# Optimization experiments

Measured on AMD Instinct MI355X. Metric: run time of the kernel, lower is better.

## Reference

```python
import jax, jax.numpy as jnp
import numpy as np

N = 50000      # nodes
E = 800000     # edges (avg degree 16)
F_IN = 512     # num_feature
H = 256        # nhid


def setup_inputs() -> dict:
    key = jax.random.key(0)
    ks = jax.random.split(key, 40)
    def p(k, shape):
        return jax.random.normal(k, shape, jnp.float32) * 0.05
    inp = {}
    inp["x"] = jax.random.normal(ks[0], (N, F_IN), jnp.float32)
    src = jax.random.randint(ks[1], (E,), 0, N, jnp.int32)
    dst = jax.random.randint(ks[2], (E,), 0, N, jnp.int32)
    inp["edge_index"] = jnp.stack([src, dst])  # [2, E]
    # GIN conv MLPs: Lin(din,H), ReLU, Lin(H,H). Weights stored [in, out].
    dims = [F_IN, H, H, H]
    i = 3
    for li, din in enumerate(dims, 1):
        inp[f"c{li}w1"] = p(ks[i], (din, H)); i += 1
        inp[f"c{li}b1"] = p(ks[i], (H,)); i += 1
        inp[f"c{li}w2"] = p(ks[i], (H, H)); i += 1
        inp[f"c{li}b2"] = p(ks[i], (H,)); i += 1
    # 2-layer LSTM, gate order i,f,g,o; single fused bias (b_ih + b_hh).
    for l in range(2):
        inp[f"lstm{l}_wih"] = p(ks[i], (H, 4 * H)); i += 1
        inp[f"lstm{l}_whh"] = p(ks[i], (H, 4 * H)); i += 1
        inp[f"lstm{l}_b"] = p(ks[i], (4 * H,)); i += 1
    inp["mlp_w"] = p(ks[i], (H, H)); i += 1
    inp["mlp_b"] = p(ks[i], (H,))
    return inp


def _gin(h, src, dst, w1, b1, w2, b2):
    # GINConv with eps=0: nn(x + sum_{j->i} x_j)
    agg = jax.ops.segment_sum(h[src], dst, num_segments=N)
    z = jax.nn.relu((h + agg) @ w1 + b1)
    return z @ w2 + b2


def _lstm_layer(seq, wih, whh, b):
    # seq: [T, N, H] -> hidden states [T, N, H]
    def step(carry, xt):
        h, c = carry
        g = xt @ wih + h @ whh + b
        i, f, gg, o = jnp.split(g, 4, axis=-1)
        c = jax.nn.sigmoid(f) * c + jax.nn.sigmoid(i) * jnp.tanh(gg)
        h = jax.nn.sigmoid(o) * jnp.tanh(c)
        return (h, c), h
    h0 = jnp.zeros((seq.shape[1], whh.shape[0]), seq.dtype)
    _, hs = jax.lax.scan(step, (h0, h0), seq)
    return hs


def reference(x, edge_index, c1w1, c1b1, c1w2, c1b2, c2w1, c2b1, c2w2, c2b2,
              c3w1, c3b1, c3w2, c3b2, c4w1, c4b1, c4w2, c4b2,
              lstm0_wih, lstm0_whh, lstm0_b, lstm1_wih, lstm1_whh, lstm1_b,
              mlp_w, mlp_b):
    src, dst = edge_index[0], edge_index[1]
    x1 = jax.nn.relu(_gin(x, src, dst, c1w1, c1b1, c1w2, c1b2))
    x2 = jax.nn.relu(_gin(x1, src, dst, c2w1, c2b1, c2w2, c2b2))
    x3 = jax.nn.relu(_gin(x2, src, dst, c3w1, c3b1, c3w2, c3b2))
    x4 = jax.nn.relu(_gin(x3, src, dst, c4w1, c4b1, c4w2, c4b2))
    # residual sums (in-place cascade as in the original)
    x2 = x2 + x1
    x3 = x3 + x2
    x4 = x4 + x3
    x_sum = x1 + x2 + x3 + x4
    stack = jnp.stack([x_sum, x1, x2, x3, x4])  # [5, N, H]
    x_avg = stack.mean(axis=0)
    x_max = stack.max(axis=0)
    seq = jnp.stack([x1, x2, x3, x4])  # [4, N, H]
    h = _lstm_layer(seq, lstm0_wih, lstm0_whh, lstm0_b)
    h = _lstm_layer(h, lstm1_wih, lstm1_whh, lstm1_b)
    x_lstm = h.mean(axis=0)
    # channel attention: relu(mlp(x_avg) + mlp(x_max) + mlp(x_lstm))
    return jax.nn.relu((x_avg + x_max + x_lstm) @ mlp_w + 3.0 * mlp_b)
```

## Files before the change

### kernel.cpp

```cpp
#include <hip/hip_runtime.h>

typedef unsigned int u32;
typedef unsigned short u16;

typedef __attribute__((ext_vector_type(8))) __bf16 bf16x8;
typedef __attribute__((ext_vector_type(4))) float f32x4;

__device__ __forceinline__ u16 f2bf(float f) {
  u32 u = __float_as_uint(f);
  u += 0x7fffu + ((u >> 16) & 1u);
  return (u16)(u >> 16);
}
__device__ __forceinline__ float bl(u32 u) { return __uint_as_float(u << 16); }
__device__ __forceinline__ float bh(u32 u) { return __uint_as_float(u & 0xffff0000u); }
__device__ __forceinline__ u32 pk2(float a, float b) { return (u32)f2bf(a) | ((u32)f2bf(b) << 16); }
__device__ __forceinline__ float fsig(float x) { return 1.f / (1.f + __expf(-x)); }
__device__ __forceinline__ float ftanh(float x) { return 1.f - 2.f / (__expf(2.f * x) + 1.f); }

#define GLDS16(gp, lp)                                                                  \
  __builtin_amdgcn_global_load_lds((const __attribute__((address_space(1))) u32*)(gp),  \
                                   (__attribute__((address_space(3))) u32*)(lp), 16, 0, 0)

struct WTargs {
  const float* src[13];
  u16* dst[13];
  int K[13];
  int Nc[13];
  int bstart[14];
};
__global__ __launch_bounds__(256) void k_wtall(WTargs wa) {
  int b = blockIdx.x;
  int w = 0;
  while (b >= wa.bstart[w + 1]) ++w;
  int i = (b - wa.bstart[w]) * 256 + threadIdx.x;
  int K = wa.K[w], Nc = wa.Nc[w];
  if (i >= K * Nc) return;
  int k = i / Nc, c = i - k * Nc;
  wa.dst[w][(size_t)c * K + k] = f2bf(wa.src[w][i]);
}

__global__ __launch_bounds__(256) void k_x2bf(const float* __restrict__ x, u16* __restrict__ xb, int total8) {
  int i = blockIdx.x * 256 + threadIdx.x;
  if (i >= total8) return;
  size_t o = (size_t)i * 8;
  float4 a = *(const float4*)(x + o), b = *(const float4*)(x + o + 4);
  uint4 v;
  v.x = pk2(a.x, a.y); v.y = pk2(a.z, a.w); v.z = pk2(b.x, b.y); v.w = pk2(b.z, b.w);
  *(uint4*)(xb + o) = v;
}

__global__ void k_hist(const int* __restrict__ dst, int* __restrict__ deg, int E) {
  int e = blockIdx.x * 256 + threadIdx.x;
  if (e < E) atomicAdd(&deg[dst[e]], 1);
}
__global__ __launch_bounds__(1024) void k_scan1(const int* __restrict__ deg, int* __restrict__ rs,
                                                int* __restrict__ bsum, int n) {
  __shared__ int buf[1024];
  int t = threadIdx.x, idx = blockIdx.x * 1024 + t;
  int v = idx < n ? deg[idx] : 0;
  buf[t] = v;
  __syncthreads();
  for (int off = 1; off < 1024; off <<= 1) {
    int u = t >= off ? buf[t - off] : 0;
    __syncthreads();
    buf[t] += u;
    __syncthreads();
  }
  if (idx < n) rs[idx + 1] = buf[t];
  if (t == 1023) bsum[blockIdx.x] = buf[1023];
}
__global__ void k_scan2(int* bsum, int nb) {
  if (threadIdx.x == 0) {
    int s = 0;
    for (int b = 0; b < nb; ++b) { s += bsum[b]; bsum[b] = s; }
  }
}
__global__ void k_scan3(const int* __restrict__ bsum, int* __restrict__ rs,
                        int* __restrict__ cursor, int n) {
  int i = blockIdx.x * 256 + threadIdx.x;
  if (i >= n) return;
  int b = i >> 10;
  int add = b ? bsum[b - 1] : 0;
  int v = rs[i + 1] + add;
  int d = cursor[i];
  rs[i + 1] = v;
  cursor[i] = v - d;
  if (i == 0) rs[0] = 0;
}
__global__ void k_scatter(const int* __restrict__ src, const int* __restrict__ dst,
                          int* __restrict__ cursor, int* __restrict__ esrc, int E) {
  int e = blockIdx.x * 256 + threadIdx.x;
  if (e < E) {
    int p = atomicAdd(&cursor[dst[e]], 1);
    esrc[p] = src[e];
  }
}

__global__ __launch_bounds__(256) void k_aggbr(const u16* __restrict__ y, const int* __restrict__ rowstart,
                                               const int* __restrict__ esrc, const float* __restrict__ b1,
                                               u16* __restrict__ z, int Nn, int base, int rows) {
  int lane = threadIdx.x & 63, wid = threadIdx.x >> 6;
  int r = blockIdx.x * 4 + wid;
  if (r >= rows) return;
  int node = base + r;
  const int cb = lane * 4;
  u16* orow = z + (size_t)r * 256 + cb;
  if (node >= Nn) { *(uint2*)orow = uint2{0, 0}; return; }
  float acc[4];
  {
    uint2 v = *(const uint2*)(y + (size_t)node * 256 + cb);
    acc[0] = bl(v.x); acc[1] = bh(v.x); acc[2] = bl(v.y); acc[3] = bh(v.y);
  }
  int s = rowstart[node], e = rowstart[node + 1];
  int j = s;
  for (; j + 3 < e; j += 4) {
    uint2 v0 = *(const uint2*)(y + (size_t)esrc[j] * 256 + cb);
    uint2 v1 = *(const uint2*)(y + (size_t)esrc[j + 1] * 256 + cb);
    uint2 v2 = *(const uint2*)(y + (size_t)esrc[j + 2] * 256 + cb);
    uint2 v3 = *(const uint2*)(y + (size_t)esrc[j + 3] * 256 + cb);
    acc[0] += (bl(v0.x) + bl(v1.x)) + (bl(v2.x) + bl(v3.x));
    acc[1] += (bh(v0.x) + bh(v1.x)) + (bh(v2.x) + bh(v3.x));
    acc[2] += (bl(v0.y) + bl(v1.y)) + (bl(v2.y) + bl(v3.y));
    acc[3] += (bh(v0.y) + bh(v1.y)) + (bh(v2.y) + bh(v3.y));
  }
  for (; j < e; ++j) {
    uint2 v = *(const uint2*)(y + (size_t)esrc[j] * 256 + cb);
    acc[0] += bl(v.x); acc[1] += bh(v.x); acc[2] += bl(v.y); acc[3] += bh(v.y);
  }
  float4 bb = *(const float4*)(b1 + cb);
  acc[0] = fmaxf(acc[0] + bb.x, 0.f);
  acc[1] = fmaxf(acc[1] + bb.y, 0.f);
  acc[2] = fmaxf(acc[2] + bb.z, 0.f);
  acc[3] = fmaxf(acc[3] + bb.w, 0.f);
  uint2 o;
  o.x = pk2(acc[0], acc[1]); o.y = pk2(acc[2], acc[3]);
  *(uint2*)orow = o;
}

__global__ __launch_bounds__(256) void k_agg256(const u16* __restrict__ h,
                                                const int* __restrict__ rowstart,
                                                const int* __restrict__ esrc,
                                                u16* __restrict__ out, int Nn, int base, int rows) {
  int lane = threadIdx.x & 63, wid = threadIdx.x >> 6;
  int r = blockIdx.x * 4 + wid;
  if (r >= rows) return;
  int node = base + r;
  const int cb = lane * 4;
  u16* orow = out + (size_t)r * 256 + cb;
  if (node >= Nn) { *(uint2*)orow = uint2{0, 0}; return; }
  float acc[4];
  {
    uint2 v = *(const uint2*)(h + (size_t)node * 256 + cb);
    acc[0] = bl(v.x); acc[1] = bh(v.x); acc[2] = bl(v.y); acc[3] = bh(v.y);
  }
  int s = rowstart[node], e = rowstart[node + 1];
  int j = s;
  for (; j + 3 < e; j += 4) {
    uint2 v0 = *(const uint2*)(h + (size_t)esrc[j] * 256 + cb);
    uint2 v1 = *(const uint2*)(h + (size_t)esrc[j + 1] * 256 + cb);
    uint2 v2 = *(const uint2*)(h + (size_t)esrc[j + 2] * 256 + cb);
    uint2 v3 = *(const uint2*)(h + (size_t)esrc[j + 3] * 256 + cb);
    acc[0] += (bl(v0.x) + bl(v1.x)) + (bl(v2.x) + bl(v3.x));
    acc[1] += (bh(v0.x) + bh(v1.x)) + (bh(v2.x) + bh(v3.x));
    acc[2] += (bl(v0.y) + bl(v1.y)) + (bl(v2.y) + bl(v3.y));
    acc[3] += (bh(v0.y) + bh(v1.y)) + (bh(v2.y) + bh(v3.y));
  }
  for (; j < e; ++j) {
    uint2 v = *(const uint2*)(h + (size_t)esrc[j] * 256 + cb);
    acc[0] += bl(v.x); acc[1] += bh(v.x); acc[2] += bl(v.y); acc[3] += bh(v.y);
  }
  uint2 o;
  o.x = pk2(acc[0], acc[1]); o.y = pk2(acc[2], acc[3]);
  *(uint2*)orow = o;
}

template <int BN, int MODE>
__global__ __launch_bounds__(256) void k_gemm(const u16* __restrict__ A1, const u16* __restrict__ B1, int K1,
                                              const u16* __restrict__ A2, const u16* __restrict__ B2, int K2,
                                              const float* __restrict__ bias, float bscale,
                                              void* __restrict__ outp, int Nout, int Mstore, int NT,
                                              u16* __restrict__ cstp, float* __restrict__ hsump,
                                              int first, int dosum) {
  constexpr int NF = BN / 32;
  __shared__ u16 Al[128 * 64];
  __shared__ u16 Bl[BN * 64];
  const int tid = threadIdx.x;
  const int lane = tid & 63, wid = tid >> 6;
  const int wr = wid >> 1, wc = wid & 1;
  const int nwg = gridDim.x;
  const int orig = blockIdx.x;
  const int q = nwg >> 3, rr8 = nwg & 7;
  const int xcd = orig & 7;
  const int wgid = (xcd < rr8 ? xcd * (q + 1) : rr8 * (q + 1) + (xcd - rr8) * q) + (orig >> 3);
  const int mtile = wgid / NT, ntile = wgid - mtile * NT;
  const int m0 = mtile * 128;
  const int n0 = ntile * BN;
  const int h0 = ntile * 32;
  const int l15 = lane & 15, l4 = lane >> 4;
  const int srow = lane >> 3;
  const int scol = ((lane & 7) ^ (lane >> 3)) * 8;
  const int rsw = l15 & 7;
  f32x4 acc[4][NF] = {};

  for (int s = 0; s < 2; ++s) {
    const u16* A = s ? A2 : A1;
    const u16* B = s ? B2 : B1;
    const int K = s ? K2 : K1;
    if (A == nullptr) continue;
    for (int k0 = 0; k0 < K; k0 += 64) {
      __syncthreads();
#pragma unroll
      for (int p = 0; p < 4; ++p) {
        int r = m0 + p * 32 + wid * 8 + srow;
        GLDS16(A + (size_t)r * K + k0 + scol, &Al[(p * 32 + wid * 8) * 64]);
      }
#pragma unroll
      for (int p = 0; p < NF; ++p) {
        int r;
        if constexpr (MODE == 3) r = p * 256 + h0 + wid * 8 + srow;
        else r = n0 + p * 32 + wid * 8 + srow;
        GLDS16(B + (size_t)r * K + k0 + scol, &Bl[(p * 32 + wid * 8) * 64]);
      }
      __syncthreads();
#pragma unroll
      for (int ks = 0; ks < 2; ++ks) {
        const int sp = (((ks * 4 + l4) ^ rsw)) * 8;
        bf16x8 af[4], bfr[NF];
#pragma unroll
        for (int m = 0; m < 4; ++m)
          af[m] = *(const bf16x8*)&Al[(wr * 64 + m * 16 + l15) * 64 + sp];
#pragma unroll
        for (int n = 0; n < NF; ++n) {
          int trow;
          if constexpr (MODE == 3) trow = n * 32 + wc * 16 + l15;
          else trow = wc * (BN / 2) + n * 16 + l15;
          bfr[n] = *(const bf16x8*)&Bl[trow * 64 + sp];
        }
#pragma unroll
        for (int m = 0; m < 4; ++m)
#pragma unroll
          for (int n = 0; n < NF; ++n)
            acc[m][n] = __builtin_amdgcn_mfma_f32_16x16x32_bf16(af[m], bfr[n], acc[m][n], 0, 0, 0);
      }
    }
  }

  if constexpr (MODE == 3) {
    const int hcol = h0 + wc * 16 + l15;
    const float bi = bias[hcol], bf2 = bias[256 + hcol];
    const float bg = bias[512 + hcol], bo = bias[768 + hcol];
    u16* hout = (u16*)outp;
#pragma unroll
    for (int m = 0; m < 4; ++m) {
      int gr0 = m0 + wr * 64 + m * 16 + l4 * 4;
#pragma unroll
      for (int r = 0; r < 4; ++r) {
        int gr = gr0 + r;
        if (gr >= Mstore) continue;
        float gi = acc[m][0][r] + bi;
        float gf = acc[m][1][r] + bf2;
        float gg = acc[m][2][r] + bg;
        float go = acc[m][3][r] + bo;
        size_t o = (size_t)gr * 256 + hcol;
        float nc = fsig(gi) * ftanh(gg);
        if (!first) nc += fsig(gf) * bl((u32)cstp[o]);
        cstp[o] = f2bf(nc);
        nc = bl((u32)f2bf(nc));
        float h = fsig(go) * ftanh(nc);
        hout[o] = f2bf(h);
        if (dosum) {
          if (first) hsump[o] = h;
          else hsump[o] += h;
        }
      }
    }
    return;
  }

#pragma unroll
  for (int m = 0; m < 4; ++m) {
    int gr0 = m0 + wr * 64 + m * 16 + l4 * 4;
#pragma unroll
    for (int n = 0; n < NF; ++n) {
      int gc = n0 + wc * (BN / 2) + n * 16 + l15;
      float bb = bias ? bias[gc] * bscale : 0.f;
#pragma unroll
      for (int r = 0; r < 4; ++r) {
        int gr = gr0 + r;
        if (gr >= Mstore) continue;
        float v = acc[m][n][r] + bb;
        if (MODE >= 1) v = fmaxf(v, 0.f);
        if (MODE == 2) ((float*)outp)[(size_t)gr * Nout + gc] = v;
        else ((u16*)outp)[(size_t)gr * Nout + gc] = f2bf(v);
      }
    }
  }
}

__global__ __launch_bounds__(256) void k_cascade(const u16* __restrict__ x1, u16* __restrict__ x2,
                                                 u16* __restrict__ x3, u16* __restrict__ x4, int total4) {
  int i = blockIdx.x * 256 + threadIdx.x;
  if (i >= total4) return;
  size_t o = (size_t)i * 4;
  uint2 v1 = *(const uint2*)(x1 + o), v2 = *(const uint2*)(x2 + o);
  uint2 v3 = *(const uint2*)(x3 + o), v4 = *(const uint2*)(x4 + o);
  float a1[4] = {bl(v1.x), bh(v1.x), bl(v1.y), bh(v1.y)};
  float a2[4] = {bl(v2.x), bh(v2.x), bl(v2.y), bh(v2.y)};
  float a3[4] = {bl(v3.x), bh(v3.x), bl(v3.y), bh(v3.y)};
  float a4[4] = {bl(v4.x), bh(v4.x), bl(v4.y), bh(v4.y)};
  float y2[4], y3[4], y4[4];
#pragma unroll
  for (int j = 0; j < 4; ++j) {
    y2[j] = a2[j] + a1[j];
    y3[j] = a3[j] + y2[j];
    y4[j] = a4[j] + y3[j];
  }
  *(uint2*)(x2 + o) = uint2{pk2(y2[0], y2[1]), pk2(y2[2], y2[3])};
  *(uint2*)(x3 + o) = uint2{pk2(y3[0], y3[1]), pk2(y3[2], y3[3])};
  *(uint2*)(x4 + o) = uint2{pk2(y4[0], y4[1]), pk2(y4[2], y4[3])};
}

__global__ __launch_bounds__(256) void k_sfin(const u16* __restrict__ x1, const u16* __restrict__ x2,
                                              const u16* __restrict__ x3, const u16* __restrict__ x4,
                                              const float* __restrict__ hsum, u16* __restrict__ sb,
                                              int total4) {
  int i = blockIdx.x * 256 + threadIdx.x;
  if (i >= total4) return;
  size_t o = (size_t)i * 4;
  uint2 v1 = *(const uint2*)(x1 + o), v2 = *(const uint2*)(x2 + o);
  uint2 v3 = *(const uint2*)(x3 + o), v4 = *(const uint2*)(x4 + o);
  float4 hh = *(const float4*)(hsum + o);
  float r0 = 1.4f * (bl(v1.x) + bl(v2.x) + bl(v3.x) + bl(v4.x)) + 0.25f * hh.x;
  float r1 = 1.4f * (bh(v1.x) + bh(v2.x) + bh(v3.x) + bh(v4.x)) + 0.25f * hh.y;
  float r2 = 1.4f * (bl(v1.y) + bl(v2.y) + bl(v3.y) + bl(v4.y)) + 0.25f * hh.z;
  float r3 = 1.4f * (bh(v1.y) + bh(v2.y) + bh(v3.y) + bh(v4.y)) + 0.25f * hh.w;
  *(uint2*)(sb + o) = uint2{pk2(r0, r1), pk2(r2, r3)};
}

extern "C" void kernel_launch(void* const* d_in, const int* in_sizes, int n_in,
                              void* d_out, int out_size, void* d_ws, size_t ws_size,
                              hipStream_t stream) {
  (void)n_in; (void)out_size;
  const int N = in_sizes[0] / 512;
  const int E = in_sizes[1] / 2;
  const int Mpad = ((N + 127) / 128) * 128;
  auto al128 = [](int v) { return ((v + 127) / 128) * 128; };

  const float* x = (const float*)d_in[0];
  const int* ei = (const int*)d_in[1];
  const int* esrc_in = ei;
  const int* edst_in = ei + E;

  size_t off = 0;
  auto alloc = [&](size_t bytes) { size_t o = off; off += (bytes + 255) & ~(size_t)255; return o; };
  char* ws = (char*)d_ws;
  const size_t szH = (size_t)Mpad * 256 * 2;
  const size_t szXB = (size_t)Mpad * 512 * 2;
  const int widx[13] = {2, 4, 6, 8, 10, 12, 14, 16, 18, 19, 21, 22, 24};
  const int wK[13] = {512, 256, 256, 256, 256, 256, 256, 256, 256, 256, 256, 256, 256};
  const int wN[13] = {256, 256, 256, 256, 256, 256, 256, 256, 1024, 1024, 1024, 1024, 256};
  size_t wt_o[13];
  for (int i = 0; i < 13; ++i) wt_o[i] = alloc((size_t)wK[i] * wN[i] * 2);
  size_t rowstart_o = alloc((size_t)(N + 1) * 4);
  size_t cursor_o = alloc((size_t)N * 4);
  size_t bsum_o = alloc(256 * 4);
  size_t esrc_o = alloc((size_t)E * 4);
  size_t x_o[4];
  for (int t = 0; t < 4; ++t) x_o[t] = alloc(szH);
  int McC = al128((Mpad + 3) / 4);
  int McL = al128((Mpad + 7) / 8);
  {
    const int ccand[3] = {Mpad, al128((Mpad + 1) / 2), al128((Mpad + 3) / 4)};
    const int lcand[5] = {Mpad, al128((Mpad + 1) / 2), 16384, 8192, al128((Mpad + 7) / 8)};
    bool done = false;
    for (int ci = 0; ci < 3 && !done; ++ci) {
      for (int li = 0; li < 5 && !done; ++li) {
        size_t cneed = szXB + szH + (size_t)ccand[ci] * 512;
        size_t lneed = (size_t)lcand[li] * 5120;
        size_t tmp = cneed > lneed ? cneed : lneed;
        if (off + tmp + (1u << 20) <= ws_size) { McC = ccand[ci]; McL = lcand[li]; done = true; }
      }
    }
  }
  const size_t hb = (size_t)McL * 256 * 2;
  const size_t fb = (size_t)McL * 256 * 4;
  size_t lstm_sz = 8 * hb + fb;
  size_t conv_sz = szXB + szH + (size_t)McC * 512;
  size_t tmp_o = alloc(lstm_sz > conv_sz ? lstm_sz : conv_sz);
  if (off > ws_size) return;

  u16* wt[13];
  for (int i = 0; i < 13; ++i) wt[i] = (u16*)(ws + wt_o[i]);
  int* rowstart = (int*)(ws + rowstart_o);
  int* cursor = (int*)(ws + cursor_o);
  int* bsum = (int*)(ws + bsum_o);
  int* esrc = (int*)(ws + esrc_o);
  u16* xl[4];
  for (int t = 0; t < 4; ++t) xl[t] = (u16*)(ws + x_o[t]);
  u16* xb = (u16*)(ws + tmp_o);
  u16* y1 = (u16*)(ws + tmp_o + szXB);
  u16* zC = (u16*)(ws + tmp_o + szXB + szH);
  u16* h0s[4];
  for (int t = 0; t < 4; ++t) h0s[t] = (u16*)(ws + tmp_o + t * hb);
  u16* h1p[2] = {(u16*)(ws + tmp_o + 4 * hb), (u16*)(ws + tmp_o + 5 * hb)};
  u16* cst = (u16*)(ws + tmp_o + 6 * hb);
  u16* sbc = (u16*)(ws + tmp_o + 7 * hb);
  float* hsum = (float*)(ws + tmp_o + 8 * hb);

  WTargs wa;
  int bacc = 0;
  for (int i = 0; i < 13; ++i) {
    wa.src[i] = (const float*)d_in[widx[i]];
    wa.dst[i] = wt[i];
    wa.K[i] = wK[i];
    wa.Nc[i] = wN[i];
    wa.bstart[i] = bacc;
    bacc += (wK[i] * wN[i] + 255) / 256;
  }
  wa.bstart[13] = bacc;
  k_wtall<<<bacc, 256, 0, stream>>>(wa);
  k_x2bf<<<(N * 64 + 255) / 256, 256, 0, stream>>>(x, xb, N * 64);
  if (Mpad > N) hipMemsetAsync(xb + (size_t)N * 512, 0, (size_t)(Mpad - N) * 512 * 2, stream);
  hipMemsetAsync(cursor, 0, (size_t)N * 4, stream);
  k_hist<<<(E + 255) / 256, 256, 0, stream>>>(edst_in, cursor, E);
  const int nb = (N + 1023) / 1024;
  k_scan1<<<nb, 1024, 0, stream>>>(cursor, rowstart, bsum, N);
  k_scan2<<<1, 64, 0, stream>>>(bsum, nb);
  k_scan3<<<(N + 255) / 256, 256, 0, stream>>>(bsum, rowstart, cursor, N);
  k_scatter<<<(E + 255) / 256, 256, 0, stream>>>(esrc_in, edst_in, cursor, esrc, E);

  auto gemm = [&](const u16* A1, const u16* B1, int K1, const u16* A2, const u16* B2, int K2,
                  const float* bias, float bscale, void* out, int Nout, int rows, int Mstore,
                  int mode) {
    dim3 b(256);
    if (mode == 0) {
      int NT = Nout / 128;
      dim3 g((rows / 128) * NT);
      k_gemm<128, 0><<<g, b, 0, stream>>>(A1, B1, K1, A2, B2, K2, bias, bscale, out, Nout, Mstore,
                                          NT, nullptr, nullptr, 0, 0);
    } else if (mode == 1) {
      int NT = Nout / 128;
      dim3 g((rows / 128) * NT);
      k_gemm<128, 1><<<g, b, 0, stream>>>(A1, B1, K1, A2, B2, K2, bias, bscale, out, Nout, Mstore,
                                          NT, nullptr, nullptr, 0, 0);
    } else {
      int NT = Nout / 64;
      dim3 g((rows / 128) * NT);
      k_gemm<64, 2><<<g, b, 0, stream>>>(A1, B1, K1, A2, B2, K2, bias, bscale, out, Nout, Mstore,
                                         NT, nullptr, nullptr, 0, 0);
    }
  };
  auto lstm_step = [&](const u16* xt, const u16* wih, const u16* hprev, const u16* whh,
                       const float* bias, u16* hout, float* hsumP, int rows, int first, int dosum) {
    dim3 g((rows / 128) * 8), b(256);
    k_gemm<128, 3><<<g, b, 0, stream>>>(xt, wih, 256, hprev, whh, 256, bias, 1.f,
                                        hout, 256, rows, 8, cst, hsumP, first, dosum);
  };

  gemm(xb, wt[0], 512, nullptr, nullptr, 0, nullptr, 0.f, y1, 256, Mpad, Mpad, 0);
  for (int base = 0; base < Mpad; base += McC) {
    int rows = Mpad - base < McC ? Mpad - base : McC;
    int ab = (rows + 3) / 4;
    k_aggbr<<<ab, 256, 0, stream>>>(y1, rowstart, esrc, (const float*)d_in[3], zC, N, base, rows);
    gemm(zC, wt[1], 256, nullptr, nullptr, 0, (const float*)d_in[5], 1.f,
         xl[0] + (size_t)base * 256, 256, rows, rows, 1);
  }
  for (int l = 1; l < 4; ++l) {
    const int cb1[4] = {3, 7, 11, 15}, cb2[4] = {5, 9, 13, 17};
    for (int base = 0; base < Mpad; base += McC) {
      int rows = Mpad - base < McC ? Mpad - base : McC;
      int ab = (rows + 3) / 4;
      k_agg256<<<ab, 256, 0, stream>>>(xl[l - 1], rowstart, esrc, zC, N, base, rows);
      gemm((u16*)zC, wt[2 * l], 256, nullptr, nullptr, 0, (const float*)d_in[cb1[l]], 1.f,
           y1, 256, rows, rows, 1);
      gemm(y1, wt[2 * l + 1], 256, nullptr, nullptr, 0, (const float*)d_in[cb2[l]], 1.f,
           xl[l] + (size_t)base * 256, 256, rows, rows, 1);
    }
  }
  k_cascade<<<(Mpad * 64 + 255) / 256, 256, 0, stream>>>(xl[0], xl[1], xl[2], xl[3], Mpad * 64);

  const float* b_l0 = (const float*)d_in[20];
  const float* b_l1 = (const float*)d_in[23];
  const float* b_mlp = (const float*)d_in[25];
  for (int base = 0; base < Mpad; base += McL) {
    int rows = Mpad - base < McL ? Mpad - base : McL;
    const size_t boff = (size_t)base * 256;
    for (int t = 0; t < 4; ++t)
      lstm_step(xl[t] + boff, wt[8], t ? h0s[t - 1] : nullptr, wt[9], b_l0,
                h0s[t], nullptr, rows, t == 0, 0);
    for (int t = 0; t < 4; ++t)
      lstm_step(h0s[t], wt[10], t ? h1p[(t + 1) & 1] : nullptr, wt[11], b_l1,
                h1p[t & 1], hsum, rows, t == 0, 1);
    k_sfin<<<(rows * 64 + 255) / 256, 256, 0, stream>>>(xl[0] + boff, xl[1] + boff, xl[2] + boff,
                                                        xl[3] + boff, hsum, sbc, rows * 64);
    int st = N - base;
    if (st > rows) st = rows;
    if (st > 0)
      gemm(sbc, wt[12], 256, nullptr, nullptr, 0, b_mlp, 3.f,
           (float*)d_out + boff, 256, rows, st, 2);
  }
}
```

Measured before the change: 1.436 ms.

## Use 256-row tiles for LSTM gemm, bf16 hidden-sum buffer, larger LSTM chunks

Templates the gemm on the M tile size and runs the fused LSTM step gemm with 256-row tiles, so each weight tile loaded into LDS is reused across twice as many rows. The running LSTM hidden-state sum is stored in bf16 instead of fp32, which cuts its memory traffic and workspace. The LSTM row-chunk candidates are changed to allow larger or full-size chunks, which means fewer launches. The cost is higher register and LDS use per block, lower occupancy, and bf16 rounding on the accumulated hidden sum.

```diff
diff --git a/kernel.cpp b/kernel.cpp
--- a/kernel.cpp
+++ b/kernel.cpp
@@ -174,15 +174,16 @@
   *(uint2*)orow = o;
 }
 
-template <int BN, int MODE>
+template <int BM, int BN, int MODE>
 __global__ __launch_bounds__(256) void k_gemm(const u16* __restrict__ A1, const u16* __restrict__ B1, int K1,
                                               const u16* __restrict__ A2, const u16* __restrict__ B2, int K2,
                                               const float* __restrict__ bias, float bscale,
                                               void* __restrict__ outp, int Nout, int Mstore, int NT,
-                                              u16* __restrict__ cstp, float* __restrict__ hsump,
+                                              u16* __restrict__ cstp, u16* __restrict__ hsump,
                                               int first, int dosum) {
+  constexpr int MF = BM / 32;
   constexpr int NF = BN / 32;
-  __shared__ u16 Al[128 * 64];
+  __shared__ u16 Al[BM * 64];
   __shared__ u16 Bl[BN * 64];
   const int tid = threadIdx.x;
   const int lane = tid & 63, wid = tid >> 6;
@@ -193,14 +194,14 @@
   const int xcd = orig & 7;
   const int wgid = (xcd < rr8 ? xcd * (q + 1) : rr8 * (q + 1) + (xcd - rr8) * q) + (orig >> 3);
   const int mtile = wgid / NT, ntile = wgid - mtile * NT;
-  const int m0 = mtile * 128;
+  const int m0 = mtile * BM;
   const int n0 = ntile * BN;
   const int h0 = ntile * 32;
   const int l15 = lane & 15, l4 = lane >> 4;
   const int srow = lane >> 3;
   const int scol = ((lane & 7) ^ (lane >> 3)) * 8;
   const int rsw = l15 & 7;
-  f32x4 acc[4][NF] = {};
+  f32x4 acc[MF][NF] = {};
 
   for (int s = 0; s < 2; ++s) {
     const u16* A = s ? A2 : A1;
@@ -210,7 +211,7 @@
     for (int k0 = 0; k0 < K; k0 += 64) {
       __syncthreads();
 #pragma unroll
-      for (int p = 0; p < 4; ++p) {
+      for (int p = 0; p < MF; ++p) {
         int r = m0 + p * 32 + wid * 8 + srow;
         GLDS16(A + (size_t)r * K + k0 + scol, &Al[(p * 32 + wid * 8) * 64]);
       }
@@ -225,10 +226,10 @@
 #pragma unroll
       for (int ks = 0; ks < 2; ++ks) {
         const int sp = (((ks * 4 + l4) ^ rsw)) * 8;
-        bf16x8 af[4], bfr[NF];
-#pragma unroll
-        for (int m = 0; m < 4; ++m)
-          af[m] = *(const bf16x8*)&Al[(wr * 64 + m * 16 + l15) * 64 + sp];
+        bf16x8 af[MF], bfr[NF];
+#pragma unroll
+        for (int m = 0; m < MF; ++m)
+          af[m] = *(const bf16x8*)&Al[(wr * (BM / 2) + m * 16 + l15) * 64 + sp];
 #pragma unroll
         for (int n = 0; n < NF; ++n) {
           int trow;
@@ -237,7 +238,7 @@
           bfr[n] = *(const bf16x8*)&Bl[trow * 64 + sp];
         }
 #pragma unroll
-        for (int m = 0; m < 4; ++m)
+        for (int m = 0; m < MF; ++m)
 #pragma unroll
           for (int n = 0; n < NF; ++n)
             acc[m][n] = __builtin_amdgcn_mfma_f32_16x16x32_bf16(af[m], bfr[n], acc[m][n], 0, 0, 0);
@@ -251,8 +252,8 @@
     const float bg = bias[512 + hcol], bo = bias[768 + hcol];
     u16* hout = (u16*)outp;
 #pragma unroll
-    for (int m = 0; m < 4; ++m) {
-      int gr0 = m0 + wr * 64 + m * 16 + l4 * 4;
+    for (int m = 0; m < MF; ++m) {
+      int gr0 = m0 + wr * (BM / 2) + m * 16 + l4 * 4;
 #pragma unroll
       for (int r = 0; r < 4; ++r) {
         int gr = gr0 + r;
@@ -269,8 +270,8 @@
         float h = fsig(go) * ftanh(nc);
         hout[o] = f2bf(h);
         if (dosum) {
-          if (first) hsump[o] = h;
-          else hsump[o] += h;
+          if (first) hsump[o] = f2bf(h);
+          else hsump[o] = f2bf(bl((u32)hsump[o]) + h);
         }
       }
     }
@@ -278,8 +279,8 @@
   }
 
 #pragma unroll
-  for (int m = 0; m < 4; ++m) {
-    int gr0 = m0 + wr * 64 + m * 16 + l4 * 4;
+  for (int m = 0; m < MF; ++m) {
+    int gr0 = m0 + wr * (BM / 2) + m * 16 + l4 * 4;
 #pragma unroll
     for (int n = 0; n < NF; ++n) {
       int gc = n0 + wc * (BN / 2) + n * 16 + l15;
@@ -322,18 +323,19 @@
 
 __global__ __launch_bounds__(256) void k_sfin(const u16* __restrict__ x1, const u16* __restrict__ x2,
                                               const u16* __restrict__ x3, const u16* __restrict__ x4,
-                                              const float* __restrict__ hsum, u16* __restrict__ sb,
+                                              const u16* __restrict__ hsum, u16* __restrict__ sb,
                                               int total4) {
   int i = blockIdx.x * 256 + threadIdx.x;
   if (i >= total4) return;
   size_t o = (size_t)i * 4;
   uint2 v1 = *(const uint2*)(x1 + o), v2 = *(const uint2*)(x2 + o);
   uint2 v3 = *(const uint2*)(x3 + o), v4 = *(const uint2*)(x4 + o);
-  float4 hh = *(const float4*)(hsum + o);
-  float r0 = 1.4f * (bl(v1.x) + bl(v2.x) + bl(v3.x) + bl(v4.x)) + 0.25f * hh.x;
-  float r1 = 1.4f * (bh(v1.x) + bh(v2.x) + bh(v3.x) + bh(v4.x)) + 0.25f * hh.y;
-  float r2 = 1.4f * (bl(v1.y) + bl(v2.y) + bl(v3.y) + bl(v4.y)) + 0.25f * hh.z;
-  float r3 = 1.4f * (bh(v1.y) + bh(v2.y) + bh(v3.y) + bh(v4.y)) + 0.25f * hh.w;
+  uint2 vh = *(const uint2*)(hsum + o);
+  float hh[4] = {bl(vh.x), bh(vh.x), bl(vh.y), bh(vh.y)};
+  float r0 = 1.4f * (bl(v1.x) + bl(v2.x) + bl(v3.x) + bl(v4.x)) + 0.25f * hh[0];
+  float r1 = 1.4f * (bh(v1.x) + bh(v2.x) + bh(v3.x) + bh(v4.x)) + 0.25f * hh[1];
+  float r2 = 1.4f * (bl(v1.y) + bl(v2.y) + bl(v3.y) + bl(v4.y)) + 0.25f * hh[2];
+  float r3 = 1.4f * (bh(v1.y) + bh(v2.y) + bh(v3.y) + bh(v4.y)) + 0.25f * hh[3];
   *(uint2*)(sb + o) = uint2{pk2(r0, r1), pk2(r2, r3)};
 }
 
@@ -343,7 +345,7 @@
   (void)n_in; (void)out_size;
   const int N = in_sizes[0] / 512;
   const int E = in_sizes[1] / 2;
-  const int Mpad = ((N + 127) / 128) * 128;
+  const int Mpad = ((N + 255) / 256) * 256;
   auto al128 = [](int v) { return ((v + 127) / 128) * 128; };
 
   const float* x = (const float*)d_in[0];
@@ -368,23 +370,22 @@
   size_t x_o[4];
   for (int t = 0; t < 4; ++t) x_o[t] = alloc(szH);
   int McC = al128((Mpad + 3) / 4);
-  int McL = al128((Mpad + 7) / 8);
+  int McL = Mpad;
   {
     const int ccand[3] = {Mpad, al128((Mpad + 1) / 2), al128((Mpad + 3) / 4)};
-    const int lcand[5] = {Mpad, al128((Mpad + 1) / 2), 16384, 8192, al128((Mpad + 7) / 8)};
+    const int lcand[5] = {Mpad, 25088, 16384, 8192, 6400};
     bool done = false;
     for (int ci = 0; ci < 3 && !done; ++ci) {
       for (int li = 0; li < 5 && !done; ++li) {
         size_t cneed = szXB + szH + (size_t)ccand[ci] * 512;
-        size_t lneed = (size_t)lcand[li] * 5120;
+        size_t lneed = (size_t)lcand[li] * 4608;
         size_t tmp = cneed > lneed ? cneed : lneed;
         if (off + tmp + (1u << 20) <= ws_size) { McC = ccand[ci]; McL = lcand[li]; done = true; }
       }
     }
   }
   const size_t hb = (size_t)McL * 256 * 2;
-  const size_t fb = (size_t)McL * 256 * 4;
-  size_t lstm_sz = 8 * hb + fb;
+  size_t lstm_sz = 9 * hb;
   size_t conv_sz = szXB + szH + (size_t)McC * 512;
   size_t tmp_o = alloc(lstm_sz > conv_sz ? lstm_sz : conv_sz);
   if (off > ws_size) return;
@@ -405,7 +406,7 @@
   u16* h1p[2] = {(u16*)(ws + tmp_o + 4 * hb), (u16*)(ws + tmp_o + 5 * hb)};
   u16* cst = (u16*)(ws + tmp_o + 6 * hb);
   u16* sbc = (u16*)(ws + tmp_o + 7 * hb);
-  float* hsum = (float*)(ws + tmp_o + 8 * hb);
+  u16* hsum = (u16*)(ws + tmp_o + 8 * hb);
 
   WTargs wa;
   int bacc = 0;
@@ -436,25 +437,25 @@
     if (mode == 0) {
       int NT = Nout / 128;
       dim3 g((rows / 128) * NT);
-      k_gemm<128, 0><<<g, b, 0, stream>>>(A1, B1, K1, A2, B2, K2, bias, bscale, out, Nout, Mstore,
-                                          NT, nullptr, nullptr, 0, 0);
+      k_gemm<128, 128, 0><<<g, b, 0, stream>>>(A1, B1, K1, A2, B2, K2, bias, bscale, out, Nout,
+                                               Mstore, NT, nullptr, nullptr, 0, 0);
     } else if (mode == 1) {
       int NT = Nout / 128;
       dim3 g((rows / 128) * NT);
-      k_gemm<128, 1><<<g, b, 0, stream>>>(A1, B1, K1, A2, B2, K2, bias, bscale, out, Nout, Mstore,
-                                          NT, nullptr, nullptr, 0, 0);
+      k_gemm<128, 128, 1><<<g, b, 0, stream>>>(A1, B1, K1, A2, B2, K2, bias, bscale, out, Nout,
+                                               Mstore, NT, nullptr, nullptr, 0, 0);
     } else {
       int NT = Nout / 64;
       dim3 g((rows / 128) * NT);
-      k_gemm<64, 2><<<g, b, 0, stream>>>(A1, B1, K1, A2, B2, K2, bias, bscale, out, Nout, Mstore,
-                                         NT, nullptr, nullptr, 0, 0);
+      k_gemm<128, 64, 2><<<g, b, 0, stream>>>(A1, B1, K1, A2, B2, K2, bias, bscale, out, Nout,
+                                              Mstore, NT, nullptr, nullptr, 0, 0);
     }
   };
   auto lstm_step = [&](const u16* xt, const u16* wih, const u16* hprev, const u16* whh,
-                       const float* bias, u16* hout, float* hsumP, int rows, int first, int dosum) {
-    dim3 g((rows / 128) * 8), b(256);
-    k_gemm<128, 3><<<g, b, 0, stream>>>(xt, wih, 256, hprev, whh, 256, bias, 1.f,
-                                        hout, 256, rows, 8, cst, hsumP, first, dosum);
+                       const float* bias, u16* hout, u16* hsumP, int rows, int first, int dosum) {
+    dim3 g((rows / 256) * 8), b(256);
+    k_gemm<256, 128, 3><<<g, b, 0, stream>>>(xt, wih, 256, hprev, whh, 256, bias, 1.f,
+                                             hout, 256, rows, 8, cst, hsumP, first, dosum);
   };
 
   gemm(xb, wt[0], 512, nullptr, nullptr, 0, nullptr, 0.f, y1, 256, Mpad, Mpad, 0);
```

Measured after the change: 2.337 ms. 62.8% more time.
